# Performance work log

Hardware: AMD Instinct MI355X
Metric: run time of the kernel (lower is better)

## Reference

```python
import jax, jax.numpy as jnp
import numpy as np

H = 1024      # hidden_size
NH = 16       # n_heads
DK = 64       # d_kv


def setup_inputs() -> dict:
    key = jax.random.key(0)
    k1, k2, k3, k4, k5 = jax.random.split(key, 5)
    x = jax.random.normal(k1, (4, 2048, H), dtype=jnp.float32)
    # dense1: hidden -> 3*n_heads*d_kv
    W1 = jax.random.normal(k2, (H, 3 * NH * DK), dtype=jnp.float32) / np.sqrt(H)
    b1 = jax.random.normal(k3, (3 * NH * DK,), dtype=jnp.float32) * 0.02
    # dense2: n_heads*d_kv -> hidden
    W2 = jax.random.normal(k4, (NH * DK, H), dtype=jnp.float32) / np.sqrt(NH * DK)
    b2 = jax.random.normal(k5, (H,), dtype=jnp.float32) * 0.02
    return {"x": x, "W1": W1, "b1": b1, "W2": W2, "b2": b2}


def reference(x, W1, b1, W2, b2):
    B, S, _ = x.shape
    scale = 1.0 / np.sqrt(DK)
    qkv = x @ W1 + b1                                   # [B,S,3*NH*DK]
    qkv = qkv.reshape(B, S, 3, NH, DK)
    q, k, v = jnp.moveaxis(qkv, 2, 0)                   # each [B,S,NH,DK]
    q = q.transpose(0, 2, 1, 3)                         # [B,NH,S,DK]
    k = k.transpose(0, 2, 1, 3)
    v = v.transpose(0, 2, 1, 3)
    scores = jnp.einsum('bhqd,bhkd->bhqk', q, k) * scale  # [B,NH,S,S]
    attn = jax.nn.softmax(scores, axis=-1)
    ctx = jnp.einsum('bhqk,bhkd->bhqd', attn, v)        # [B,NH,S,DK]
    ctx = ctx.transpose(0, 2, 1, 3).reshape(B, S, NH * DK)
    return ctx @ W2 + b2
```

## Files before the change

### kernel.cpp

```cpp
#include <hip/hip_runtime.h>
#include <hip/hip_bf16.h>


typedef __hip_bfloat16 bf16;
typedef __attribute__((ext_vector_type(8))) short bf16x8;
typedef __attribute__((ext_vector_type(4))) float f32x4;

#define B_   4
#define S_   2048
#define H_   1024
#define NH_  16
#define DK_  64
#define M_   8192
#define N1_  3072
#define K_   1024

#define SCALE_Q 0.18033688f

typedef const __attribute__((address_space(1))) void* gas_t;
typedef __attribute__((address_space(3))) void* las_t;
#define G2L16(g, l) __builtin_amdgcn_global_load_lds((gas_t)(g), (las_t)(l), 16, 0, 0)

#if __has_builtin(__builtin_amdgcn_exp2f)
#define EX2(x) __builtin_amdgcn_exp2f(x)
#else
#define EX2(x) exp2f(x)
#endif

__device__ __forceinline__ float b2f(bf16 v) { return __bfloat162float(v); }

__device__ __forceinline__ unsigned pk2(float a, float b) {
    unsigned ua = __float_as_uint(a);
    unsigned ub = __float_as_uint(b);
    ua += 0x7FFFu + ((ua >> 16) & 1u);
    ub += 0x7FFFu + ((ub >> 16) & 1u);
    return (ua >> 16) | (ub & 0xFFFF0000u);
}

__global__ __launch_bounds__(256) void conv_x(const float* __restrict__ X,
                                              bf16* __restrict__ Xb)
{
    size_t i = ((size_t)blockIdx.x * 256 + threadIdx.x) * 8;
    float4 lo = *(const float4*)&X[i];
    float4 hi = *(const float4*)&X[i + 4];
    uint4 u;
    u.x = pk2(lo.x, lo.y); u.y = pk2(lo.z, lo.w);
    u.z = pk2(hi.x, hi.y); u.w = pk2(hi.z, hi.w);
    *(uint4*)&Xb[i] = u;
}

__global__ __launch_bounds__(256) void conv_wT(const float* __restrict__ W,
                                               bf16* __restrict__ WT,
                                               int Kdim, int Ndim)
{
    __shared__ bf16 T[64][72];
    const int tid = threadIdx.x;
    const int n0 = blockIdx.x * 64, k0 = blockIdx.y * 64;
    const int kr = tid >> 4, nc = (tid & 15) * 4;
    #pragma unroll
    for (int p = 0; p < 4; ++p) {
        float4 v = *(const float4*)&W[(size_t)(k0 + kr + p * 16) * Ndim + n0 + nc];
        T[nc + 0][kr + p * 16] = __float2bfloat16(v.x);
        T[nc + 1][kr + p * 16] = __float2bfloat16(v.y);
        T[nc + 2][kr + p * 16] = __float2bfloat16(v.z);
        T[nc + 3][kr + p * 16] = __float2bfloat16(v.w);
    }
    __syncthreads();
    const int nr = tid >> 2, kc = (tid & 3) * 16;
    *(bf16x8*)&WT[(size_t)(n0 + nr) * Kdim + k0 + kc]     = *(const bf16x8*)&T[nr][kc];
    *(bf16x8*)&WT[(size_t)(n0 + nr) * Kdim + k0 + kc + 8] = *(const bf16x8*)&T[nr][kc + 8];
}

__device__ __forceinline__ void qkv_epilogue(
    const f32x4 acc[4][4], const float* __restrict__ B1,
    bf16* __restrict__ Qp, bf16* __restrict__ Kp, bf16* __restrict__ Vt,
    int n0, int m0, int wm, int wn, int quad, int col)
{
    const int which = n0 >> 10;
    const int bb = m0 >> 11;
    if (which == 2) {
        #pragma unroll
        for (int i = 0; i < 4; ++i) {
            int s = (m0 & (S_ - 1)) + wm * 64 + i * 16 + quad * 4;
            #pragma unroll
            for (int j = 0; j < 4; ++j) {
                int n = n0 + wn * 64 + j * 16 + col;
                int h = (n >> 6) & 15, d = n & 63;
                float bv = B1[n];
                uint2 t;
                t.x = pk2(acc[i][j][0] + bv, acc[i][j][1] + bv);
                t.y = pk2(acc[i][j][2] + bv, acc[i][j][3] + bv);
                *(uint2*)&Vt[(((size_t)(bb * NH_ + h)) * DK_ + d) * S_ + s] = t;
            }
        }
    } else {
        bf16* dst = which ? Kp : Qp;
        const float sc = which ? 1.0f : SCALE_Q;
        #pragma unroll
        for (int i = 0; i < 4; ++i) {
            #pragma unroll
            for (int r = 0; r < 4; ++r) {
                int s = (m0 & (S_ - 1)) + wm * 64 + i * 16 + quad * 4 + r;
                #pragma unroll
                for (int j = 0; j < 4; ++j) {
                    int n = n0 + wn * 64 + j * 16 + col;
                    int h = (n >> 6) & 15, d = n & 63;
                    dst[(((size_t)(bb * NH_ + h)) * S_ + s) * DK_ + d] =
                        __float2bfloat16((acc[i][j][r] + B1[n]) * sc);
                }
            }
        }
    }
}

__global__ __launch_bounds__(256) void gemm_qkv_mfma2(
    const bf16* __restrict__ Xb, const bf16* __restrict__ W1T,
    const float* __restrict__ B1,
    bf16* __restrict__ Qp, bf16* __restrict__ Kp, bf16* __restrict__ Vt)
{
    __shared__ bf16 As[128 * 32];
    __shared__ bf16 Bs[128 * 32];

    const int tid = threadIdx.x;
    const int lane = tid & 63, wv = tid >> 6;
    const int col = lane & 15, quad = lane >> 4;
    const int wm = wv >> 1, wn = wv & 1;
    const int n0 = blockIdx.x * 128, m0 = blockIdx.y * 128;

    f32x4 acc[4][4] = {};

    const bf16* Ag = Xb  + (size_t)m0 * K_;
    const bf16* Bg = W1T + (size_t)n0 * K_;

    for (int k0 = 0; k0 < K_; k0 += 32) {
        #pragma unroll
        for (int h = 0; h < 2; ++h) {
            int idx = tid + h * 256;
            int row = idx >> 2, c = (idx & 3) * 8;
            G2L16(Ag + (size_t)row * K_ + k0 + c, As + (size_t)idx * 8);
            G2L16(Bg + (size_t)row * K_ + k0 + c, Bs + (size_t)idx * 8);
        }
        __syncthreads();

        bf16x8 af[4], bfr[4];
        #pragma unroll
        for (int i = 0; i < 4; ++i)
            af[i] = *(const bf16x8*)&As[(wm * 64 + i * 16 + col) * 32 + quad * 8];
        #pragma unroll
        for (int j = 0; j < 4; ++j)
            bfr[j] = *(const bf16x8*)&Bs[(wn * 64 + j * 16 + col) * 32 + quad * 8];

        #pragma unroll
        for (int i = 0; i < 4; ++i)
            #pragma unroll
            for (int j = 0; j < 4; ++j)
                acc[i][j] = __builtin_amdgcn_mfma_f32_16x16x32_bf16(af[i], bfr[j], acc[i][j], 0, 0, 0);
        __syncthreads();
    }
    qkv_epilogue(acc, B1, Qp, Kp, Vt, n0, m0, wm, wn, quad, col);
}

__global__ __launch_bounds__(256) void gemm_qkv_mfma(
    const float* __restrict__ X, const bf16* __restrict__ W1T,
    const float* __restrict__ B1,
    bf16* __restrict__ Qp, bf16* __restrict__ Kp, bf16* __restrict__ Vt)
{
    __shared__ bf16 As[128 * 32];
    __shared__ bf16 Bs[128 * 32];

    const int tid = threadIdx.x;
    const int lane = tid & 63, wv = tid >> 6;
    const int col = lane & 15, quad = lane >> 4;
    const int wm = wv >> 1, wn = wv & 1;
    const int n0 = blockIdx.x * 128, m0 = blockIdx.y * 128;

    f32x4 acc[4][4] = {};

    const float* Ag = X   + (size_t)m0 * K_;
    const bf16*  Bg = W1T + (size_t)n0 * K_;

    for (int k0 = 0; k0 < K_; k0 += 32) {
        #pragma unroll
        for (int h = 0; h < 2; ++h) {
            int idx = tid + h * 256;
            int row = idx >> 2, c = (idx & 3) * 8;
            G2L16(Bg + (size_t)row * K_ + k0 + c, Bs + (size_t)idx * 8);
        }
        #pragma unroll
        for (int h = 0; h < 2; ++h) {
            int idx = tid + h * 256;
            int row = idx >> 2, c = (idx & 3) * 8;
            float4 lo = *(const float4*)&Ag[(size_t)row * K_ + k0 + c];
            float4 hi = *(const float4*)&Ag[(size_t)row * K_ + k0 + c + 4];
            uint4 u;
            u.x = pk2(lo.x, lo.y); u.y = pk2(lo.z, lo.w);
            u.z = pk2(hi.x, hi.y); u.w = pk2(hi.z, hi.w);
            *(uint4*)&As[(size_t)idx * 8] = u;
        }
        __syncthreads();

        bf16x8 af[4], bfr[4];
        #pragma unroll
        for (int i = 0; i < 4; ++i)
            af[i] = *(const bf16x8*)&As[(wm * 64 + i * 16 + col) * 32 + quad * 8];
        #pragma unroll
        for (int j = 0; j < 4; ++j)
            bfr[j] = *(const bf16x8*)&Bs[(wn * 64 + j * 16 + col) * 32 + quad * 8];

        #pragma unroll
        for (int i = 0; i < 4; ++i)
            #pragma unroll
            for (int j = 0; j < 4; ++j)
                acc[i][j] = __builtin_amdgcn_mfma_f32_16x16x32_bf16(af[i], bfr[j], acc[i][j], 0, 0, 0);
        __syncthreads();
    }
    qkv_epilogue(acc, B1, Qp, Kp, Vt, n0, m0, wm, wn, quad, col);
}

__global__ __launch_bounds__(256, 4) void attn_mfma(
    const bf16* __restrict__ Q, const bf16* __restrict__ K,
    const bf16* __restrict__ Vt, bf16* __restrict__ CTX)
{
    __shared__ bf16 Ks[64][72];
    __shared__ bf16 Vs[64][72];
    __shared__ bf16 Ps[4][2][16][72];

    const int tid  = threadIdx.x;
    const int wv   = tid >> 6;
    const int lane = tid & 63;
    const int col  = lane & 15;
    const int quad = lane >> 4;

    const int bh = blockIdx.y;
    const int q0 = blockIdx.x * 128;

    const bf16* Qg  = Q  + (size_t)bh * S_ * DK_;
    const bf16* Kg  = K  + (size_t)bh * S_ * DK_;
    const bf16* Vtg = Vt + (size_t)bh * DK_ * S_;

    const short oneb = (short)0x3F80;
    const bf16x8 ones = {oneb, oneb, oneb, oneb, oneb, oneb, oneb, oneb};

    bf16x8 qf[2][2];
    #pragma unroll
    for (int qs = 0; qs < 2; ++qs) {
        const int qrow = q0 + wv * 32 + qs * 16 + col;
        qf[qs][0] = *(const bf16x8*)&Qg[(size_t)qrow * DK_ + quad * 8];
        qf[qs][1] = *(const bf16x8*)&Qg[(size_t)qrow * DK_ + 32 + quad * 8];
    }

    f32x4 o[2][4] = {};
    f32x4 l_acc[2] = {};

    const int sr = tid >> 2;
    const int e0 = (tid & 3) * 16;

    bf16x8 kreg0 = *(const bf16x8*)&Kg[(size_t)sr * DK_ + e0];
    bf16x8 kreg1 = *(const bf16x8*)&Kg[(size_t)sr * DK_ + e0 + 8];
    bf16x8 vreg0 = *(const bf16x8*)&Vtg[(size_t)sr * S_ + e0];
    bf16x8 vreg1 = *(const bf16x8*)&Vtg[(size_t)sr * S_ + e0 + 8];

    for (int kt = 0; kt < S_ / 64; ++kt) {
        *(bf16x8*)&Ks[sr][e0]     = kreg0;
        *(bf16x8*)&Ks[sr][e0 + 8] = kreg1;
        *(bf16x8*)&Vs[sr][e0]     = vreg0;
        *(bf16x8*)&Vs[sr][e0 + 8] = vreg1;
        __syncthreads();

        if (kt + 1 < S_ / 64) {
            kreg0 = *(const bf16x8*)&Kg[(size_t)((kt + 1) * 64 + sr) * DK_ + e0];
            kreg1 = *(const bf16x8*)&Kg[(size_t)((kt + 1) * 64 + sr) * DK_ + e0 + 8];
            vreg0 = *(const bf16x8*)&Vtg[(size_t)sr * S_ + (kt + 1) * 64 + e0];
            vreg1 = *(const bf16x8*)&Vtg[(size_t)sr * S_ + (kt + 1) * 64 + e0 + 8];
        }

        #pragma unroll
        for (int cs = 0; cs < 4; ++cs) {
            const bf16* kb = &Ks[cs * 16 + col][0];
            bf16x8 ka0 = *(const bf16x8*)&kb[quad * 8];
            bf16x8 ka1 = *(const bf16x8*)&kb[32 + quad * 8];
            #pragma unroll
            for (int qs = 0; qs < 2; ++qs) {
                f32x4 a = {0.f, 0.f, 0.f, 0.f};
                a = __builtin_amdgcn_mfma_f32_16x16x32_bf16(ka0, qf[qs][0], a, 0, 0, 0);
                a = __builtin_amdgcn_mfma_f32_16x16x32_bf16(ka1, qf[qs][1], a, 0, 0, 0);
                uint2 p;
                p.x = pk2(EX2(a[0]), EX2(a[1]));
                p.y = pk2(EX2(a[2]), EX2(a[3]));
                *(uint2*)&Ps[wv][qs][col][cs * 16 + quad * 4] = p;
            }
        }

        bf16x8 pf[2][2];
        #pragma unroll
        for (int qs = 0; qs < 2; ++qs) {
            pf[qs][0] = *(const bf16x8*)&Ps[wv][qs][col][quad * 8];
            pf[qs][1] = *(const bf16x8*)&Ps[wv][qs][col][32 + quad * 8];
            l_acc[qs] = __builtin_amdgcn_mfma_f32_16x16x32_bf16(ones, pf[qs][0], l_acc[qs], 0, 0, 0);
            l_acc[qs] = __builtin_amdgcn_mfma_f32_16x16x32_bf16(ones, pf[qs][1], l_acc[qs], 0, 0, 0);
        }

        #pragma unroll
        for (int ds = 0; ds < 4; ++ds) {
            const bf16* vb = &Vs[ds * 16 + col][0];
            bf16x8 va0 = *(const bf16x8*)&vb[quad * 8];
            bf16x8 va1 = *(const bf16x8*)&vb[32 + quad * 8];
            #pragma unroll
            for (int qs = 0; qs < 2; ++qs) {
                o[qs][ds] = __builtin_amdgcn_mfma_f32_16x16x32_bf16(va0, pf[qs][0], o[qs][ds], 0, 0, 0);
                o[qs][ds] = __builtin_amdgcn_mfma_f32_16x16x32_bf16(va1, pf[qs][1], o[qs][ds], 0, 0, 0);
            }
        }
        __syncthreads();
    }

    const int b = bh >> 4, h = bh & 15;
    #pragma unroll
    for (int qs = 0; qs < 2; ++qs) {
        const float inv = 1.f / l_acc[qs][0];
        const int srow = q0 + wv * 32 + qs * 16 + col;
        bf16* crow = CTX + ((size_t)(b * S_ + srow)) * H_ + h * DK_;
        #pragma unroll
        for (int ds = 0; ds < 4; ++ds) {
            uint2 t;
            t.x = pk2(o[qs][ds][0] * inv, o[qs][ds][1] * inv);
            t.y = pk2(o[qs][ds][2] * inv, o[qs][ds][3] * inv);
            *(uint2*)&crow[ds * 16 + quad * 4] = t;
        }
    }
}

__global__ __launch_bounds__(256) void gemm_out_mfma(
    const bf16* __restrict__ Cx, const bf16* __restrict__ W2T,
    const float* __restrict__ B2, float* __restrict__ OUT)
{
    __shared__ bf16 As[128 * 32];
    __shared__ bf16 Bs[128 * 32];

    const int tid = threadIdx.x;
    const int lane = tid & 63, wv = tid >> 6;
    const int col = lane & 15, quad = lane >> 4;
    const int wm = wv >> 1, wn = wv & 1;
    const int n0 = blockIdx.x * 128, m0 = blockIdx.y * 128;

    f32x4 acc[4][4] = {};

    const bf16* Ag = Cx  + (size_t)m0 * K_;
    const bf16* Bg = W2T + (size_t)n0 * K_;

    for (int k0 = 0; k0 < K_; k0 += 32) {
        #pragma unroll
        for (int h = 0; h < 2; ++h) {
            int idx = tid + h * 256;
            int row = idx >> 2, c = (idx & 3) * 8;
            G2L16(Ag + (size_t)row * K_ + k0 + c, As + (size_t)idx * 8);
            G2L16(Bg + (size_t)row * K_ + k0 + c, Bs + (size_t)idx * 8);
        }
        __syncthreads();

        bf16x8 af[4], bfr[4];
        #pragma unroll
        for (int i = 0; i < 4; ++i)
            af[i] = *(const bf16x8*)&As[(wm * 64 + i * 16 + col) * 32 + quad * 8];
        #pragma unroll
        for (int j = 0; j < 4; ++j)
            bfr[j] = *(const bf16x8*)&Bs[(wn * 64 + j * 16 + col) * 32 + quad * 8];

        #pragma unroll
        for (int i = 0; i < 4; ++i)
            #pragma unroll
            for (int j = 0; j < 4; ++j)
                acc[i][j] = __builtin_amdgcn_mfma_f32_16x16x32_bf16(af[i], bfr[j], acc[i][j], 0, 0, 0);
        __syncthreads();
    }

    #pragma unroll
    for (int i = 0; i < 4; ++i) {
        #pragma unroll
        for (int r = 0; r < 4; ++r) {
            int m = m0 + wm * 64 + i * 16 + quad * 4 + r;
            #pragma unroll
            for (int j = 0; j < 4; ++j) {
                int n = n0 + wn * 64 + j * 16 + col;
                OUT[(size_t)m * H_ + n] = acc[i][j][r] + B2[n];
            }
        }
    }
}

extern "C" void kernel_launch(void* const* d_in, const int* in_sizes, int n_in,
                              void* d_out, int out_size, void* d_ws, size_t ws_size,
                              hipStream_t stream)
{
    const float* X  = (const float*)d_in[0];
    const float* W1 = (const float*)d_in[1];
    const float* B1 = (const float*)d_in[2];
    const float* W2 = (const float*)d_in[3];
    const float* B2 = (const float*)d_in[4];
    float* OUT = (float*)d_out;

    const size_t QE = (size_t)B_ * NH_ * S_ * DK_;
    bf16* Qw  = (bf16*)d_ws;
    bf16* Kw  = Qw + QE;
    bf16* Vw  = Kw + QE;
    bf16* Rw  = Vw + QE;
    bf16* W1T = Rw;
    bf16* Cw  = Rw;
    bf16* W2T = Qw;
    bf16* Xb  = Rw + QE;

    const bool fast = ws_size >= 5 * QE * sizeof(bf16);

    conv_wT<<<dim3(N1_ / 64, K_ / 64), 256, 0, stream>>>(W1, W1T, K_, N1_);
    if (fast) {
        conv_x<<<dim3((int)(QE / (256 * 8))), 256, 0, stream>>>(X, Xb);
        gemm_qkv_mfma2<<<dim3(N1_ / 128, M_ / 128), 256, 0, stream>>>(Xb, W1T, B1, Qw, Kw, Vw);
    } else {
        gemm_qkv_mfma<<<dim3(N1_ / 128, M_ / 128), 256, 0, stream>>>(X, W1T, B1, Qw, Kw, Vw);
    }
    attn_mfma<<<dim3(S_ / 128, B_ * NH_), 256, 0, stream>>>(Qw, Kw, Vw, Cw);
    conv_wT<<<dim3(H_ / 64, K_ / 64), 256, 0, stream>>>(W2, W2T, K_, H_);
    gemm_out_mfma<<<dim3(H_ / 128, M_ / 128), 256, 0, stream>>>(Cw, W2T, B2, OUT);
}
```

Before: 298.3 us.

## Keep softmax probabilities in registers and remap attention block order

Drops the LDS round trip for the probability tile. The exponentiated scores from the QK^T MFMA output layout are fed straight into 16x16x16 bf16 MFMAs for the PV product and the row-sum accumulation, and V is read per 16-key slice to match. It also remaps block indices so that consecutive blocks spread across heads, which is likely meant to improve cache locality. The cost is twice as many, smaller MFMA instructions for PV and more LDS reads of V.

```diff
diff --git a/kernel.cpp b/kernel.cpp
--- a/kernel.cpp
+++ b/kernel.cpp
@@ -4,6 +4,7 @@
 
 typedef __hip_bfloat16 bf16;
 typedef __attribute__((ext_vector_type(8))) short bf16x8;
+typedef __attribute__((ext_vector_type(4))) short bf16x4;
 typedef __attribute__((ext_vector_type(4))) float f32x4;
 
 #define B_   4
@@ -25,6 +26,12 @@
 #define EX2(x) __builtin_amdgcn_exp2f(x)
 #else
 #define EX2(x) exp2f(x)
+#endif
+
+#if __has_builtin(__builtin_amdgcn_mfma_f32_16x16x16_bf16)
+#define MFMA16(a, b, c) __builtin_amdgcn_mfma_f32_16x16x16_bf16(a, b, c, 0, 0, 0)
+#else
+#define MFMA16(a, b, c) __builtin_amdgcn_mfma_f32_16x16x16bf16_1k(a, b, c, 0, 0, 0)
 #endif
 
 __device__ __forceinline__ float b2f(bf16 v) { return __bfloat162float(v); }
@@ -223,7 +230,6 @@
 {
     __shared__ bf16 Ks[64][72];
     __shared__ bf16 Vs[64][72];
-    __shared__ bf16 Ps[4][2][16][72];
 
     const int tid  = threadIdx.x;
     const int wv   = tid >> 6;
@@ -231,15 +237,17 @@
     const int col  = lane & 15;
     const int quad = lane >> 4;
 
-    const int bh = blockIdx.y;
-    const int q0 = blockIdx.x * 128;
+    const int lid = blockIdx.x + (blockIdx.y << 4);
+    const int vid = (lid & 7) * 128 + (lid >> 3);
+    const int bh = vid >> 4;
+    const int q0 = (vid & 15) * 128;
 
     const bf16* Qg  = Q  + (size_t)bh * S_ * DK_;
     const bf16* Kg  = K  + (size_t)bh * S_ * DK_;
     const bf16* Vtg = Vt + (size_t)bh * DK_ * S_;
 
     const short oneb = (short)0x3F80;
-    const bf16x8 ones = {oneb, oneb, oneb, oneb, oneb, oneb, oneb, oneb};
+    const bf16x4 ones4 = {oneb, oneb, oneb, oneb};
 
     bf16x8 qf[2][2];
     #pragma unroll
@@ -279,36 +287,24 @@
             const bf16* kb = &Ks[cs * 16 + col][0];
             bf16x8 ka0 = *(const bf16x8*)&kb[quad * 8];
             bf16x8 ka1 = *(const bf16x8*)&kb[32 + quad * 8];
+            bf16x4 vf[4];
+            #pragma unroll
+            for (int ds = 0; ds < 4; ++ds)
+                vf[ds] = *(const bf16x4*)&Vs[ds * 16 + col][cs * 16 + quad * 4];
+
             #pragma unroll
             for (int qs = 0; qs < 2; ++qs) {
                 f32x4 a = {0.f, 0.f, 0.f, 0.f};
                 a = __builtin_amdgcn_mfma_f32_16x16x32_bf16(ka0, qf[qs][0], a, 0, 0, 0);
                 a = __builtin_amdgcn_mfma_f32_16x16x32_bf16(ka1, qf[qs][1], a, 0, 0, 0);
-                uint2 p;
-                p.x = pk2(EX2(a[0]), EX2(a[1]));
-                p.y = pk2(EX2(a[2]), EX2(a[3]));
-                *(uint2*)&Ps[wv][qs][col][cs * 16 + quad * 4] = p;
-            }
-        }
-
-        bf16x8 pf[2][2];
-        #pragma unroll
-        for (int qs = 0; qs < 2; ++qs) {
-            pf[qs][0] = *(const bf16x8*)&Ps[wv][qs][col][quad * 8];
-            pf[qs][1] = *(const bf16x8*)&Ps[wv][qs][col][32 + quad * 8];
-            l_acc[qs] = __builtin_amdgcn_mfma_f32_16x16x32_bf16(ones, pf[qs][0], l_acc[qs], 0, 0, 0);
-            l_acc[qs] = __builtin_amdgcn_mfma_f32_16x16x32_bf16(ones, pf[qs][1], l_acc[qs], 0, 0, 0);
-        }
-
-        #pragma unroll
-        for (int ds = 0; ds < 4; ++ds) {
-            const bf16* vb = &Vs[ds * 16 + col][0];
-            bf16x8 va0 = *(const bf16x8*)&vb[quad * 8];
-            bf16x8 va1 = *(const bf16x8*)&vb[32 + quad * 8];
-            #pragma unroll
-            for (int qs = 0; qs < 2; ++qs) {
-                o[qs][ds] = __builtin_amdgcn_mfma_f32_16x16x32_bf16(va0, pf[qs][0], o[qs][ds], 0, 0, 0);
-                o[qs][ds] = __builtin_amdgcn_mfma_f32_16x16x32_bf16(va1, pf[qs][1], o[qs][ds], 0, 0, 0);
+                union { uint2 u; bf16x4 h; } cv;
+                cv.u.x = pk2(EX2(a[0]), EX2(a[1]));
+                cv.u.y = pk2(EX2(a[2]), EX2(a[3]));
+                const bf16x4 pb = cv.h;
+                l_acc[qs] = MFMA16(ones4, pb, l_acc[qs]);
+                #pragma unroll
+                for (int ds = 0; ds < 4; ++ds)
+                    o[qs][ds] = MFMA16(vf[ds], pb, o[qs][ds]);
             }
         }
         __syncthreads();
```

After: 295.6 us. Within noise of the previous version (-0.9%).
